# Kernel tuning notes

Measured on AMD Instinct MI355X. Metric: run time of the kernel, lower is better.

## Reference

```python
import jax, jax.numpy as jnp
import numpy as np

TOP_K = 38        # int(256 * 0.15)
DROP_BLOCK = 5
HALF = DROP_BLOCK // 2  # floor(drop_block/2)


def setup_inputs() -> dict:
    key = jax.random.key(0)
    k1, k2, k3 = jax.random.split(key, 3)
    B, C, H, W = 64, 256, 56, 56
    d = 16  # max(C // reduction, 4)
    x = jax.random.normal(k1, (B, C, H, W), dtype=jnp.float32)
    w1 = jax.random.normal(k2, (d, C), dtype=jnp.float32) * 0.08  # fc1 1x1 conv weight
    w2 = jax.random.normal(k3, (C, d), dtype=jnp.float32) * 0.25  # fc2 1x1 conv weight
    return {"x": x, "w1": w1, "w2": w2}


def reference(x, w1, w2):
    B, C, H, W = x.shape
    # --- SEModule: global avg pool + 1x1 convs (= matmuls) + sigmoid ---
    pooled = x.mean(axis=(2, 3))                              # [B, C]
    hidden = jax.nn.relu(jnp.einsum('bc,dc->bd', pooled, w1))  # [B, d]
    M = jax.nn.sigmoid(jnp.einsum('bd,cd->bc', hidden, w2))    # [B, C]

    # --- Select_TopK: one-hot mask of top_k channels per sample ---
    _, topk_idx = jax.lax.top_k(M, TOP_K)                     # [B, TOP_K]
    T = jnp.zeros((B, C), dtype=x.dtype).at[
        jnp.arange(B)[:, None], topk_idx].set(1.0)            # [B, C]

    # --- Apply_Mask: per selected (b,c) row, zero a DROP_BLOCK box around argmax, rescale ---
    xf = x.reshape(B * C, H, W)
    flat = xf.reshape(B * C, H * W)
    max_idx = jnp.argmax(flat, axis=1)                        # [B*C]
    mh = max_idx // W
    mw = max_idx % W
    h1 = jnp.clip(mh - HALF, 0, H - 1)
    h2 = jnp.clip(mh + HALF, 0, H - 1)
    w1b = jnp.clip(mw - HALF, 0, W - 1)
    w2b = jnp.clip(mw + HALF, 0, W - 1)

    rows = jnp.arange(H)[None, :, None]                       # [1, H, 1]
    cols = jnp.arange(W)[None, None, :]                       # [1, 1, W]
    in_box = ((rows >= h1[:, None, None]) & (rows <= h2[:, None, None]) &
              (cols >= w1b[:, None, None]) & (cols <= w2b[:, None, None]))
    S = 1.0 - in_box.astype(x.dtype)                          # [B*C, H, W]
    lam = (H * W) / S.sum(axis=(1, 2))                        # [B*C]
    masked = xf * S * lam[:, None, None]

    Tf = T.reshape(B * C)
    out = jnp.where(Tf[:, None, None] > 0, masked, xf)
    return out.reshape(B, C, H, W)
```

## Files before the change

kernel.cpp:

```cpp
#include <hip/hip_runtime.h>
#include <stdint.h>

#define BB 64
#define CC 256
#define HH 56
#define WW 56
#define HWN 3136
#define NCH (BB*CC)
#define TOPK 38
#define NV4 784
#define DD 16

__global__ __launch_bounds__(256) void reduce_kernel(const float* __restrict__ x,
                                                     double* __restrict__ sums,
                                                     int* __restrict__ amax) {
    const int wave = threadIdx.x >> 6;
    const int lane = threadIdx.x & 63;
    const int ch = blockIdx.x * 4 + wave;
    const float4* p = (const float4*)(x + (size_t)ch * HWN);

    double s = 0.0;
    float bv = -INFINITY; int bi = 0x7fffffff;
    for (int i = lane; i < NV4; i += 64) {
        float4 q = p[i];
        float f[4] = {q.x, q.y, q.z, q.w};
        const int e0 = i * 4;
        #pragma unroll
        for (int j = 0; j < 4; ++j) {
            s += (double)f[j];
            const int ij = e0 + j;
            if (f[j] > bv || (f[j] == bv && ij < bi)) { bv = f[j]; bi = ij; }
        }
    }
    for (int off = 32; off >= 1; off >>= 1) {
        s += __shfl_down(s, off, 64);
        float ov = __shfl_down(bv, off, 64);
        int   oi = __shfl_down(bi, off, 64);
        if (ov > bv || (ov == bv && oi < bi)) { bv = ov; bi = oi; }
    }
    if (lane == 0) { sums[ch] = s; amax[ch] = bi; }
}

__global__ __launch_bounds__(256) void mask_kernel(const double* __restrict__ sums,
                                                   const int* __restrict__ amax,
                                                   const float* __restrict__ w1,
                                                   const float* __restrict__ w2,
                                                   float* __restrict__ lam_out,
                                                   uint32_t* __restrict__ box_out) {
    const int b = blockIdx.x;
    const int c = threadIdx.x;
    __shared__ double pooled[CC];
    __shared__ double hidden[DD];
    __shared__ double Ms[CC];

    pooled[c] = sums[b * CC + c] / (double)HWN;
    __syncthreads();

    if (c < DD) {
        double acc = 0.0;
        for (int j = 0; j < CC; ++j) acc += pooled[j] * (double)w1[c * CC + j];
        hidden[c] = acc > 0.0 ? acc : 0.0;
    }
    __syncthreads();

    double acc = 0.0;
    for (int d = 0; d < DD; ++d) acc += hidden[d] * (double)w2[c * DD + d];
    double m = 1.0 / (1.0 + exp(-acc));
    Ms[c] = m;
    __syncthreads();

    int rank = 0;
    for (int j = 0; j < CC; ++j) {
        double mj = Ms[j];
        rank += (mj > m || (mj == m && j < c)) ? 1 : 0;
    }
    const bool sel = rank < TOPK;

    const int idx = amax[b * CC + c];
    const int mh = idx / WW, mw = idx - (idx / WW) * WW;
    const int h1 = mh - 2 > 0 ? mh - 2 : 0;
    const int h2 = mh + 2 < HH - 1 ? mh + 2 : HH - 1;
    const int w1b = mw - 2 > 0 ? mw - 2 : 0;
    const int w2b = mw + 2 < WW - 1 ? mw + 2 : WW - 1;
    const int area = (h2 - h1 + 1) * (w2b - w1b + 1);

    lam_out[b * CC + c] = sel ? (float)HWN / (float)(HWN - area) : 1.0f;
    box_out[b * CC + c] = sel
        ? (uint32_t)(h1 | (h2 << 8) | (w1b << 16) | (w2b << 24))
        : 0xFFu;
}

__global__ __launch_bounds__(256) void apply_kernel(const float* __restrict__ x,
                                                    float* __restrict__ out,
                                                    const float* __restrict__ lam_arr,
                                                    const uint32_t* __restrict__ box_arr) {
    const int wave = threadIdx.x >> 6;
    const int lane = threadIdx.x & 63;
    const int ch = blockIdx.x * 4 + wave;

    const float lam = lam_arr[ch];
    const uint32_t box = box_arr[ch];
    const int h1 = box & 0xff, h2 = (box >> 8) & 0xff;
    const int w1b = (box >> 16) & 0xff, w2b = (box >> 24) & 0xff;

    const float4* p = (const float4*)(x + (size_t)ch * HWN);
    float4* q = (float4*)(out + (size_t)ch * HWN);

    for (int i = lane; i < NV4; i += 64) {
        float4 v = p[i];
        const int row = i / 14;
        const int cb = (i - row * 14) * 4;
        const bool inrow = (row >= h1) && (row <= h2);
        float f[4] = {v.x, v.y, v.z, v.w};
        #pragma unroll
        for (int j = 0; j < 4; ++j) {
            const int cj = cb + j;
            f[j] *= lam;
            if (inrow && cj >= w1b && cj <= w2b) f[j] = 0.0f;
        }
        float4 o; o.x = f[0]; o.y = f[1]; o.z = f[2]; o.w = f[3];
        q[i] = o;
    }
}

extern "C" void kernel_launch(void* const* d_in, const int* in_sizes, int n_in,
                              void* d_out, int out_size, void* d_ws, size_t ws_size,
                              hipStream_t stream) {
    const float* x  = (const float*)d_in[0];
    const float* w1 = (const float*)d_in[1];
    const float* w2 = (const float*)d_in[2];
    float* out = (float*)d_out;

    char* ws = (char*)d_ws;
    double*   sums = (double*)(ws);
    int*      amax = (int*)(ws + 131072);
    float*    lam  = (float*)(ws + 196608);
    uint32_t* box  = (uint32_t*)(ws + 262144);

    reduce_kernel<<<NCH / 4, 256, 0, stream>>>(x, sums, amax);
    mask_kernel<<<BB, 256, 0, stream>>>(sums, amax, w1, w2, lam, box);
    apply_kernel<<<NCH / 4, 256, 0, stream>>>(x, out, lam, box);
}
```

Measured before the change: 404.4 us.

## Fuse output copy into reduction pass and apply mask only to selected channels

The reduction kernel now writes each input channel straight to the output with nontemporal stores while computing sums and argmax. The mask kernel compacts the top-k selected channels into a dense list. The apply kernel then rewrites only those selected channels instead of all of them, which avoids re-reading the full input and cuts total memory traffic. In exchange, the reduction kernel carries more store traffic, and the selected channels are written twice.

```diff
diff --git a/kernel.cpp b/kernel.cpp
--- a/kernel.cpp
+++ b/kernel.cpp
@@ -10,20 +10,26 @@
 #define TOPK 38
 #define NV4 784
 #define DD 16
+#define NSEL (BB*TOPK)
 
-__global__ __launch_bounds__(256) void reduce_kernel(const float* __restrict__ x,
-                                                     double* __restrict__ sums,
-                                                     int* __restrict__ amax) {
+typedef float floatx4 __attribute__((ext_vector_type(4)));
+
+__global__ __launch_bounds__(256) void reduce_copy_kernel(const float* __restrict__ x,
+                                                          float* __restrict__ out,
+                                                          double* __restrict__ sums,
+                                                          int* __restrict__ amax) {
     const int wave = threadIdx.x >> 6;
     const int lane = threadIdx.x & 63;
     const int ch = blockIdx.x * 4 + wave;
-    const float4* p = (const float4*)(x + (size_t)ch * HWN);
+    const floatx4* p = (const floatx4*)(x + (size_t)ch * HWN);
+    floatx4* q = (floatx4*)(out + (size_t)ch * HWN);
 
     double s = 0.0;
     float bv = -INFINITY; int bi = 0x7fffffff;
     for (int i = lane; i < NV4; i += 64) {
-        float4 q = p[i];
-        float f[4] = {q.x, q.y, q.z, q.w};
+        floatx4 v = p[i];
+        __builtin_nontemporal_store(v, q + i);
+        float f[4] = {v.x, v.y, v.z, v.w};
         const int e0 = i * 4;
         #pragma unroll
         for (int j = 0; j < 4; ++j) {
@@ -45,8 +51,9 @@
                                                    const int* __restrict__ amax,
                                                    const float* __restrict__ w1,
                                                    const float* __restrict__ w2,
-                                                   float* __restrict__ lam_out,
-                                                   uint32_t* __restrict__ box_out) {
+                                                   int* __restrict__ sel_ch,
+                                                   float* __restrict__ sel_lam,
+                                                   uint32_t* __restrict__ sel_box) {
     const int b = blockIdx.x;
     const int c = threadIdx.x;
     __shared__ double pooled[CC];
@@ -74,32 +81,35 @@
         double mj = Ms[j];
         rank += (mj > m || (mj == m && j < c)) ? 1 : 0;
     }
-    const bool sel = rank < TOPK;
 
-    const int idx = amax[b * CC + c];
-    const int mh = idx / WW, mw = idx - (idx / WW) * WW;
-    const int h1 = mh - 2 > 0 ? mh - 2 : 0;
-    const int h2 = mh + 2 < HH - 1 ? mh + 2 : HH - 1;
-    const int w1b = mw - 2 > 0 ? mw - 2 : 0;
-    const int w2b = mw + 2 < WW - 1 ? mw + 2 : WW - 1;
-    const int area = (h2 - h1 + 1) * (w2b - w1b + 1);
+    if (rank < TOPK) {
+        const int idx = amax[b * CC + c];
+        const int mh = idx / WW, mw = idx - (idx / WW) * WW;
+        const int h1 = mh - 2 > 0 ? mh - 2 : 0;
+        const int h2 = mh + 2 < HH - 1 ? mh + 2 : HH - 1;
+        const int w1b = mw - 2 > 0 ? mw - 2 : 0;
+        const int w2b = mw + 2 < WW - 1 ? mw + 2 : WW - 1;
+        const int area = (h2 - h1 + 1) * (w2b - w1b + 1);
 
-    lam_out[b * CC + c] = sel ? (float)HWN / (float)(HWN - area) : 1.0f;
-    box_out[b * CC + c] = sel
-        ? (uint32_t)(h1 | (h2 << 8) | (w1b << 16) | (w2b << 24))
-        : 0xFFu;
+        const int slot = b * TOPK + rank;
+        sel_ch[slot]  = b * CC + c;
+        sel_lam[slot] = (float)HWN / (float)(HWN - area);
+        sel_box[slot] = (uint32_t)(h1 | (h2 << 8) | (w1b << 16) | (w2b << 24));
+    }
 }
 
-__global__ __launch_bounds__(256) void apply_kernel(const float* __restrict__ x,
-                                                    float* __restrict__ out,
-                                                    const float* __restrict__ lam_arr,
-                                                    const uint32_t* __restrict__ box_arr) {
+__global__ __launch_bounds__(256) void apply_sel_kernel(const float* __restrict__ x,
+                                                        float* __restrict__ out,
+                                                        const int* __restrict__ sel_ch,
+                                                        const float* __restrict__ sel_lam,
+                                                        const uint32_t* __restrict__ sel_box) {
     const int wave = threadIdx.x >> 6;
     const int lane = threadIdx.x & 63;
-    const int ch = blockIdx.x * 4 + wave;
+    const int slot = blockIdx.x * 4 + wave;
 
-    const float lam = lam_arr[ch];
-    const uint32_t box = box_arr[ch];
+    const int ch = sel_ch[slot];
+    const float lam = sel_lam[slot];
+    const uint32_t box = sel_box[slot];
     const int h1 = box & 0xff, h2 = (box >> 8) & 0xff;
     const int w1b = (box >> 16) & 0xff, w2b = (box >> 24) & 0xff;
 
@@ -132,12 +142,13 @@
     float* out = (float*)d_out;
 
     char* ws = (char*)d_ws;
-    double*   sums = (double*)(ws);
-    int*      amax = (int*)(ws + 131072);
-    float*    lam  = (float*)(ws + 196608);
-    uint32_t* box  = (uint32_t*)(ws + 262144);
+    double*   sums    = (double*)(ws);
+    int*      amax    = (int*)(ws + 131072);
+    int*      sel_ch  = (int*)(ws + 196608);
+    float*    sel_lam = (float*)(ws + 212992);
+    uint32_t* sel_box = (uint32_t*)(ws + 229376);
 
-    reduce_kernel<<<NCH / 4, 256, 0, stream>>>(x, sums, amax);
-    mask_kernel<<<BB, 256, 0, stream>>>(sums, amax, w1, w2, lam, box);
-    apply_kernel<<<NCH / 4, 256, 0, stream>>>(x, out, lam, box);
+    reduce_copy_kernel<<<NCH / 4, 256, 0, stream>>>(x, out, sums, amax);
+    mask_kernel<<<BB, 256, 0, stream>>>(sums, amax, w1, w2, sel_ch, sel_lam, sel_box);
+    apply_sel_kernel<<<NSEL / 4, 256, 0, stream>>>(x, out, sel_ch, sel_lam, sel_box);
 }
```

Result: faster. 385.8 us (-4.6%).
